# Kernel tuning notes

Hardware: AMD Instinct MI355X
Metric: run time of the kernel (lower is better)

The kernel has to match this reference:

```python
import jax, jax.numpy as jnp
import numpy as np

H = 2048          # hidden size
N_HEADS = 16
HEAD_DIM = H // N_HEADS   # 128
ATTN_SCALE = 8.0          # attention_scale > 1.0 -> custom max-subtract path
B, S = 2, 2048


def setup_inputs() -> dict:
    key = jax.random.key(0)
    k1, k2, k3, k4, k5 = jax.random.split(key, 5)
    hidden_states = jax.random.normal(k1, (B, S, H), dtype=jnp.float32)
    # causal left-to-right multiplicative mask, broadcast over batch and heads
    ltor_mask = jnp.tril(jnp.ones((S, S), dtype=jnp.float32))[None, None]
    std = 0.02
    W_qkv = jax.random.normal(k2, (H, 3 * H), dtype=jnp.float32) * std
    b_qkv = jnp.zeros((3 * H,), dtype=jnp.float32)
    W_out = jax.random.normal(k3, (H, H), dtype=jnp.float32) * std
    b_out = jnp.zeros((H,), dtype=jnp.float32)
    return {"hidden_states": hidden_states, "ltor_mask": ltor_mask,
            "W_qkv": W_qkv, "b_qkv": b_qkv, "W_out": W_out, "b_out": b_out}


def reference(hidden_states, ltor_mask, W_qkv, b_qkv, W_out, b_out):
    b, s, h = hidden_states.shape
    # fused QKV projection: [b, s, 3h]
    qkv = jnp.einsum('bsh,hk->bsk', hidden_states, W_qkv) + b_qkv
    q, k, v = jnp.split(qkv, 3, axis=-1)
    # [b, s, h] -> [b, n, s, hn]
    def to_heads(t):
        return t.reshape(b, s, N_HEADS, HEAD_DIM).transpose(0, 2, 1, 3)
    q, k, v = to_heads(q), to_heads(k), to_heads(v)
    # custom scale: q / sqrt(scale), k / sqrt(hn * scale)
    inv = 1.0 / (ATTN_SCALE * np.sqrt(np.float32(HEAD_DIM)))
    scores = jnp.einsum('bnqd,bnkd->bnqk', q, k) * jnp.float32(inv)
    # multiplicative mask BEFORE max-subtract (zeroes masked positions)
    scores = scores * ltor_mask
    # attention_scale > 1.0 path: subtract row max, re-multiply by scale
    scores = (scores - jnp.max(scores, axis=-1, keepdims=True)) * jnp.float32(ATTN_SCALE)
    # additive large-negative fill on masked entries
    scores = scores + jnp.float32(-65504.0) * (1.0 - ltor_mask)
    probs = jax.nn.softmax(scores, axis=-1)
    ctx = jnp.einsum('bnqk,bnkd->bnqd', probs, v)
    ctx = ctx.transpose(0, 2, 1, 3).reshape(b, s, h)
    out = jnp.einsum('bsh,hk->bsk', ctx, W_out) + b_out
    return out
```

## Files before the change

kernel.cpp:

```cpp
#include <hip/hip_runtime.h>

#define S_LEN 2048
#define HDIM  2048
#define NHEADS 16
#define DHEAD 128
#define BATCH 2
#define MROWS (BATCH * S_LEN)
#define QKVN  (3 * HDIM)

typedef _Float16 f16;
typedef _Float16 f16x8 __attribute__((ext_vector_type(8)));
typedef _Float16 f16x4 __attribute__((ext_vector_type(4)));
typedef float    f32x4 __attribute__((ext_vector_type(4)));
typedef float    f32x16 __attribute__((ext_vector_type(16)));

typedef const __attribute__((address_space(1))) void* gas_ptr;
typedef __attribute__((address_space(3))) void*       las_ptr;

#define MFMA16(a, b, c)  __builtin_amdgcn_mfma_f32_16x16x32_f16(a, b, c, 0, 0, 0)
#define MFMA32(a, b, c)  __builtin_amdgcn_mfma_f32_32x32x16_f16(a, b, c, 0, 0, 0)

__device__ __forceinline__ void gl_lds16(const f16* g, f16* lds_wave_base) {
#if defined(__has_builtin) && __has_builtin(__builtin_amdgcn_global_load_lds)
  __builtin_amdgcn_global_load_lds((gas_ptr)g, (las_ptr)lds_wave_base, 16, 0, 0);
#else
  int lane = threadIdx.x & 63;
  ((f16x8*)lds_wave_base)[lane] = *(const f16x8*)g;
#endif
}


__global__ __launch_bounds__(256) void cvt_blocked_kernel(const float* __restrict__ X,
                                                          f16* __restrict__ Xb) {
  int kt = blockIdx.x;
  int rt = blockIdx.y;
  int t = threadIdx.x;
  int m = t >> 1, half = t & 1;
  const float* src = X + (size_t)(rt * 128 + m) * HDIM + kt * 32 + half * 16;
  float4 v0 = ((const float4*)src)[0];
  float4 v1 = ((const float4*)src)[1];
  float4 v2 = ((const float4*)src)[2];
  float4 v3 = ((const float4*)src)[3];
  f16x8 a = {(f16)v0.x, (f16)v0.y, (f16)v0.z, (f16)v0.w,
             (f16)v1.x, (f16)v1.y, (f16)v1.z, (f16)v1.w};
  f16x8 b = {(f16)v2.x, (f16)v2.y, (f16)v2.z, (f16)v2.w,
             (f16)v3.x, (f16)v3.y, (f16)v3.z, (f16)v3.w};
  f16* dst = Xb + ((size_t)rt * 64 + kt) * 4096 + ((half * 2) * 128 + m) * 8;
  *(f16x8*)dst = a;
  *(f16x8*)(dst + 1024) = b;
}

__global__ __launch_bounds__(256) void transpose_cvt_blocked_kernel(
    const float* __restrict__ W, f16* __restrict__ Wb, int K, int N) {
  __shared__ float tile[64][65];
  int k0 = blockIdx.y * 64, n0 = blockIdx.x * 64;
  int tr = threadIdx.x >> 4;
  int tc = (threadIdx.x & 15) * 4;
  int KT = K >> 5;
#pragma unroll
  for (int rr = 0; rr < 4; ++rr) {
    int r = rr * 16 + tr;
    float4 v = *(const float4*)(W + (size_t)(k0 + r) * N + n0 + tc);
    tile[r][tc + 0] = v.x; tile[r][tc + 1] = v.y;
    tile[r][tc + 2] = v.z; tile[r][tc + 3] = v.w;
  }
  __syncthreads();
#pragma unroll
  for (int rr = 0; rr < 4; ++rr) {
    int r = rr * 16 + tr;
    int n = n0 + r;
    int kBase = k0 + tc;
    f16x4 o;
#pragma unroll
    for (int c = 0; c < 4; ++c) o[c] = (f16)tile[tc + c][r];
    int nt = n >> 7, nn = n & 127;
    int kt = kBase >> 5, kc = (kBase >> 3) & 3, j = kBase & 7;
    *(f16x4*)(Wb + ((size_t)nt * KT + kt) * 4096 + (kc * 128 + nn) * 8 + j) = o;
  }
}

template <int MODE>
__global__ __launch_bounds__(256) void gemm_kernel(const f16* __restrict__ Ablk,
                                                   const f16* __restrict__ Bblk,
                                                   const float* __restrict__ bias,
                                                   f16* __restrict__ Cpart,
                                                   f16* __restrict__ Qr,
                                                   f16* __restrict__ KB,
                                                   f16* __restrict__ VB,
                                                   int M, int N, int K) {
  __shared__ f16 As[4 * 128 * 8];
  __shared__ f16 Bs[4 * 128 * 8];
  int tid = threadIdx.x;
  int lane = tid & 63, w = tid >> 6;
  int lhi = lane >> 4, llo = lane & 15;
  int m0 = blockIdx.y * 128, n0 = blockIdx.x * 128;
  int wm = (w & 1) * 64, wn = (w >> 1) * 64;
  int KT = K >> 5;
  const f16* Ab = Ablk + (size_t)blockIdx.y * KT * 4096;
  const f16* Bb = Bblk + (size_t)blockIdx.x * KT * 4096;

  int ktBeg = 0, ktEnd = KT;
  if (MODE == 2) { int half = KT >> 1; ktBeg = blockIdx.z * half; ktEnd = ktBeg + half; }

  f32x4 acc[4][4];
#pragma unroll
  for (int i = 0; i < 4; ++i)
#pragma unroll
    for (int j = 0; j < 4; ++j) acc[i][j] = (f32x4){0.f, 0.f, 0.f, 0.f};

  for (int kt = ktBeg; kt < ktEnd; ++kt) {
    __syncthreads();
#pragma unroll
    for (int i2 = 0; i2 < 2; ++i2) {
      int Lw = i2 * 256 + w * 64;
      gl_lds16(Ab + (size_t)kt * 4096 + Lw * 8 + (lane * 8), As + Lw * 8);
      gl_lds16(Bb + (size_t)kt * 4096 + Lw * 8 + (lane * 8), Bs + Lw * 8);
    }
    __syncthreads();

    f16x8 af[4], bf[4];
#pragma unroll
    for (int i = 0; i < 4; ++i)
      af[i] = *(const f16x8*)(As + (lhi * 128 + wm + i * 16 + llo) * 8);
#pragma unroll
    for (int j = 0; j < 4; ++j)
      bf[j] = *(const f16x8*)(Bs + (lhi * 128 + wn + j * 16 + llo) * 8);
#pragma unroll
    for (int i = 0; i < 4; ++i)
#pragma unroll
      for (int j = 0; j < 4; ++j) acc[i][j] = MFMA16(af[i], bf[j], acc[i][j]);
  }

#pragma unroll
  for (int j = 0; j < 4; ++j) {
    int col = n0 + wn + j * 16 + llo;
    float bv = (MODE == 1) ? bias[col] : 0.f;
#pragma unroll
    for (int i = 0; i < 4; ++i) {
      int rowb = m0 + wm + i * 16 + lhi * 4;
      if (MODE == 2) {
        size_t zoff = (size_t)blockIdx.z * M * N;
#pragma unroll
        for (int r = 0; r < 4; ++r)
          Cpart[zoff + (size_t)(rowb + r) * N + col] = (f16)acc[i][j][r];
      } else {
        int region = n0 >> 11;
        if (region == 0) {
#pragma unroll
          for (int r = 0; r < 4; ++r)
            Qr[(size_t)(rowb + r) * HDIM + col] = (f16)(acc[i][j][r] + bv);
        } else if (region == 1) {
          int cK = col - HDIM;
          int hd = cK >> 7, d = cK & 127, g = d >> 3, dj = d & 7;
#pragma unroll
          for (int r = 0; r < 4; ++r) {
            int row = rowb + r;
            int b = row >> 11, s = row & 2047;
            int kt2 = s >> 6, key = s & 63;
            size_t addr = ((((size_t)(b * 16 + hd) * 32 + kt2) * 16 + g) * 64 + key) * 8 + dj;
            KB[addr] = (f16)(acc[i][j][r] + bv);
          }
        } else {
          int cV = col - 2 * HDIM;
          int hd = cV >> 7, d = cV & 127;
          int row = rowb;
          int b = row >> 11, s = row & 2047;
          int kt2 = s >> 6, key = s & 63;
          int kg = key >> 3, kj = key & 7;
          f16x4 pv = {(f16)(acc[i][j][0] + bv), (f16)(acc[i][j][1] + bv),
                      (f16)(acc[i][j][2] + bv), (f16)(acc[i][j][3] + bv)};
          size_t addr = ((((size_t)(b * 16 + hd) * 32 + kt2) * 8 + kg) * 128 + d) * 8 + kj;
          *(f16x4*)(VB + addr) = pv;
        }
      }
    }
  }
}

__global__ __launch_bounds__(256) void merge_out_kernel(const f16* __restrict__ Cpart,
                                                        const float* __restrict__ bias,
                                                        float* __restrict__ out) {
  int t = blockIdx.x * 256 + threadIdx.x;
  int col8 = (t & 255) * 8;
  int row = t >> 8;
  size_t base = (size_t)row * HDIM + col8;
  const size_t MN = (size_t)MROWS * HDIM;
  f16x8 a = *(const f16x8*)(Cpart + base);
  f16x8 b = *(const f16x8*)(Cpart + MN + base);
  float4 b0 = *(const float4*)(bias + col8);
  float4 b1 = *(const float4*)(bias + col8 + 4);
  float4 o0 = {(float)a[0] + (float)b[0] + b0.x, (float)a[1] + (float)b[1] + b0.y,
               (float)a[2] + (float)b[2] + b0.z, (float)a[3] + (float)b[3] + b0.w};
  float4 o1 = {(float)a[4] + (float)b[4] + b1.x, (float)a[5] + (float)b[5] + b1.y,
               (float)a[6] + (float)b[6] + b1.z, (float)a[7] + (float)b[7] + b1.w};
  *(float4*)(out + base) = o0;
  *(float4*)(out + base + 4) = o1;
}

__global__ __launch_bounds__(256, 2) void attn_kernel(const f16* __restrict__ Qr,
                                                      const f16* __restrict__ KB,
                                                      const f16* __restrict__ VB,
                                                      f16* __restrict__ Opart,
                                                      float* __restrict__ Lpart) {
  __shared__ f16 Ks[1024 * 8];
  __shared__ f16 Vs[1024 * 8];
  __shared__ f16 Ps[4][32 * 72];

  int tid = threadIdx.x, lane = tid & 63, w = tid >> 6;
  int l5 = lane & 31, hl = lane >> 5;
  int bh = blockIdx.y, b = bh >> 4, hd = bh & 15;
  int gx = blockIdx.x;

  int g, rem;
  if (gx < 4)       { g = 0; rem = gx; }
  else if (gx < 12) { g = 1; rem = gx - 4; }
  else if (gx < 24) { g = 2; rem = gx - 12; }
  else              { g = 3; rem = gx - 24; }
  int nseg = g + 1;
  int qt = g * 4 + rem / nseg;
  int seg = rem % nseg;
  int cnt = 2 * qt + 2;
  int kt0 = seg * cnt / nseg;
  int kt1 = (seg + 1) * cnt / nseg;

  int qbase = qt * 128 + w * 32;
  int qrow = qbase + l5;

  const f16* qp = Qr + (size_t)(b * S_LEN + qrow) * HDIM + hd * DHEAD + hl * 8;
  f16x8 qf[8];
#pragma unroll
  for (int s8 = 0; s8 < 8; ++s8) qf[s8] = *(const f16x8*)(qp + s8 * 16);

  f32x16 oac[4];
#pragma unroll
  for (int mt = 0; mt < 4; ++mt)
#pragma unroll
    for (int r = 0; r < 16; ++r) oac[mt][r] = 0.f;
  float rs = 0.f;

  const float C1 = 0.12752747419986393f;
  const float C2 = 11.541560327111708f;

  const f16* KBb = KB + (size_t)bh * 32 * 8192;
  const f16* VBb = VB + (size_t)bh * 32 * 8192;

  for (int kt = kt0; kt < kt1; ++kt) {
    __syncthreads();
    {
      const f16* Kt = KBb + (size_t)kt * 8192;
      const f16* Vt = VBb + (size_t)kt * 8192;
#pragma unroll
      for (int c = 0; c < 4; ++c) {
        int u0 = w * 256 + c * 64;
        gl_lds16(Kt + (size_t)(u0 + lane) * 8, Ks + u0 * 8);
        gl_lds16(Vt + (size_t)(u0 + lane) * 8, Vs + u0 * 8);
      }
    }
    __syncthreads();

    if (kt * 64 <= qbase + 31) {
      f32x16 sac[2];
#pragma unroll
      for (int mt = 0; mt < 2; ++mt)
#pragma unroll
        for (int r = 0; r < 16; ++r) sac[mt][r] = 0.f;
#pragma unroll
      for (int s8 = 0; s8 < 8; ++s8) {
#pragma unroll
        for (int mt = 0; mt < 2; ++mt) {
          f16x8 kf = *(const f16x8*)(Ks + ((s8 * 2 + hl) * 64 + mt * 32 + l5) * 8);
          sac[mt] = MFMA32(kf, qf[s8], sac[mt]);
        }
      }

      bool diag = (kt * 64 + 63 > qbase);
#pragma unroll
      for (int mt = 0; mt < 2; ++mt) {
#pragma unroll
        for (int g4 = 0; g4 < 4; ++g4) {
          f16x4 pk;
#pragma unroll
          for (int r = 0; r < 4; ++r) {
            int keyl = mt * 32 + g4 * 8 + hl * 4 + r;
            float p = __builtin_amdgcn_exp2f(fmaf(sac[mt][g4 * 4 + r], C1, -C2));
            if (diag && (kt * 64 + keyl > qrow)) p = 0.f;
            rs += p;
            pk[r] = (f16)p;
          }
          *(f16x4*)(&Ps[w][l5 * 72 + mt * 32 + g4 * 8 + hl * 4]) = pk;
        }
      }
      asm volatile("s_waitcnt lgkmcnt(0)" ::: "memory");

#pragma unroll
      for (int ks = 0; ks < 4; ++ks) {
        f16x8 pf = *(const f16x8*)(&Ps[w][l5 * 72 + ks * 16 + hl * 8]);
#pragma unroll
        for (int mt = 0; mt < 4; ++mt) {
          f16x8 vf = *(const f16x8*)(Vs + ((ks * 2 + hl) * 128 + mt * 32 + l5) * 8);
          oac[mt] = MFMA32(vf, pf, oac[mt]);
        }
      }
    }
  }

  float lsum = rs + __shfl_xor(rs, 32, 64);
  int lq = w * 32 + l5;
  size_t slot = (size_t)bh * 40 + gx;
  size_t ob = slot * (128 * DHEAD) + (size_t)lq * DHEAD;
#pragma unroll
  for (int mt = 0; mt < 4; ++mt) {
#pragma unroll
    for (int g4 = 0; g4 < 4; ++g4) {
      int d = mt * 32 + g4 * 8 + hl * 4;
      f16x4 ov = {(f16)oac[mt][g4 * 4 + 0], (f16)oac[mt][g4 * 4 + 1],
                  (f16)oac[mt][g4 * 4 + 2], (f16)oac[mt][g4 * 4 + 3]};
      *(f16x4*)(Opart + ob + d) = ov;
    }
  }
  if (hl == 0) Lpart[slot * 128 + lq] = lsum;
}

__global__ __launch_bounds__(256) void merge_kernel(const f16* __restrict__ Opart,
                                                    const float* __restrict__ Lpart,
                                                    f16* __restrict__ CTXb) {
  int t = blockIdx.x * 256 + threadIdx.x;
  int d8 = (t & 15) * 8;
  int q = (t >> 4) & 2047;
  int bh = t >> 15;
  int b = bh >> 4, hd = bh & 15;
  int qt = q >> 7, lq = q & 127;
  int g = qt >> 2;
  int nseg = g + 1;
  int gxbase = 2 * g * (g + 1) + (qt & 3) * nseg;
  size_t slot0 = (size_t)bh * 40 + gxbase;
  float acc[8];
#pragma unroll
  for (int j = 0; j < 8; ++j) acc[j] = 0.f;
  float l = 0.f;
  for (int s = 0; s < nseg; ++s) {
    l += Lpart[(slot0 + s) * 128 + lq];
    f16x8 a = *(const f16x8*)(Opart + (slot0 + s) * (128 * DHEAD) + (size_t)lq * DHEAD + d8);
#pragma unroll
    for (int j = 0; j < 8; ++j) acc[j] += (float)a[j];
  }
  float inv = 1.0f / l;
  f16x8 o;
#pragma unroll
  for (int j = 0; j < 8; ++j) o[j] = (f16)(acc[j] * inv);
  int row = b * S_LEN + q;
  int col = hd * DHEAD + d8;
  int rt = row >> 7, rr = row & 127;
  int kt = col >> 5, kc = (col >> 3) & 3;
  *(f16x8*)(CTXb + ((size_t)rt * 64 + kt) * 4096 + (kc * 128 + rr) * 8) = o;
}

extern "C" void kernel_launch(void* const* d_in, const int* in_sizes, int n_in,
                              void* d_out, int out_size, void* d_ws, size_t ws_size,
                              hipStream_t stream) {
  const float* X    = (const float*)d_in[0];
  const float* Wqkv = (const float*)d_in[2];
  const float* bqkv = (const float*)d_in[3];
  const float* Wout = (const float*)d_in[4];
  const float* bout = (const float*)d_in[5];
  float* out = (float*)d_out;

  char* ws = (char*)d_ws;
  f16* Xb    = (f16*)ws;  ws += (size_t)MROWS * HDIM * sizeof(f16);
  f16* Wqkvb = (f16*)ws;  ws += (size_t)QKVN * HDIM * sizeof(f16);
  f16* Woutb = (f16*)ws;  ws += (size_t)HDIM * HDIM * sizeof(f16);
  f16* Qr    = (f16*)ws;  ws += (size_t)MROWS * HDIM * sizeof(f16);
  f16* KB    = (f16*)ws;  ws += (size_t)32 * 32 * 8192 * sizeof(f16);
  f16* VB    = (f16*)ws;  ws += (size_t)32 * 32 * 8192 * sizeof(f16);
  f16* Opart = (f16*)ws;  ws += (size_t)32 * 40 * 128 * DHEAD * sizeof(f16);
  float* Lpart = (float*)ws;  ws += (size_t)32 * 40 * 128 * sizeof(float);
  f16* CTXb  = Xb;
  f16* Cpart = Opart;

  cvt_blocked_kernel<<<dim3(HDIM / 32, MROWS / 128), 256, 0, stream>>>(X, Xb);
  transpose_cvt_blocked_kernel<<<dim3(QKVN / 64, HDIM / 64), 256, 0, stream>>>(Wqkv, Wqkvb, HDIM, QKVN);
  transpose_cvt_blocked_kernel<<<dim3(HDIM / 64, HDIM / 64), 256, 0, stream>>>(Wout, Woutb, HDIM, HDIM);

  gemm_kernel<1><<<dim3(QKVN / 128, MROWS / 128), 256, 0, stream>>>(
      Xb, Wqkvb, bqkv, nullptr, Qr, KB, VB, MROWS, QKVN, HDIM);

  attn_kernel<<<dim3(40, 32), 256, 0, stream>>>(Qr, KB, VB, Opart, Lpart);

  merge_kernel<<<(32 * S_LEN * 16) / 256, 256, 0, stream>>>(Opart, Lpart, CTXb);

  gemm_kernel<2><<<dim3(HDIM / 128, MROWS / 128, 2), 256, 0, stream>>>(
      CTXb, Woutb, nullptr, Cpart, nullptr, nullptr, nullptr, MROWS, HDIM, HDIM);

  merge_out_kernel<<<(MROWS * HDIM / 8) / 256, 256, 0, stream>>>(Cpart, bout, out);
}
```

Baseline: 419.0 us.

## Double-buffer K/V tiles in attention and drop split-K in output projection

```diff
diff --git a/kernel.cpp b/kernel.cpp
--- a/kernel.cpp
+++ b/kernel.cpp
@@ -83,7 +83,7 @@
 __global__ __launch_bounds__(256) void gemm_kernel(const f16* __restrict__ Ablk,
                                                    const f16* __restrict__ Bblk,
                                                    const float* __restrict__ bias,
-                                                   f16* __restrict__ Cpart,
+                                                   float* __restrict__ Cout,
                                                    f16* __restrict__ Qr,
                                                    f16* __restrict__ KB,
                                                    f16* __restrict__ VB,
@@ -99,16 +99,13 @@
   const f16* Ab = Ablk + (size_t)blockIdx.y * KT * 4096;
   const f16* Bb = Bblk + (size_t)blockIdx.x * KT * 4096;
 
-  int ktBeg = 0, ktEnd = KT;
-  if (MODE == 2) { int half = KT >> 1; ktBeg = blockIdx.z * half; ktEnd = ktBeg + half; }
-
   f32x4 acc[4][4];
 #pragma unroll
   for (int i = 0; i < 4; ++i)
 #pragma unroll
     for (int j = 0; j < 4; ++j) acc[i][j] = (f32x4){0.f, 0.f, 0.f, 0.f};
 
-  for (int kt = ktBeg; kt < ktEnd; ++kt) {
+  for (int kt = 0; kt < KT; ++kt) {
     __syncthreads();
 #pragma unroll
     for (int i2 = 0; i2 < 2; ++i2) {
@@ -134,15 +131,14 @@
 #pragma unroll
   for (int j = 0; j < 4; ++j) {
     int col = n0 + wn + j * 16 + llo;
-    float bv = (MODE == 1) ? bias[col] : 0.f;
+    float bv = bias[col];
 #pragma unroll
     for (int i = 0; i < 4; ++i) {
       int rowb = m0 + wm + i * 16 + lhi * 4;
-      if (MODE == 2) {
-        size_t zoff = (size_t)blockIdx.z * M * N;
+      if (MODE == 0) {
 #pragma unroll
         for (int r = 0; r < 4; ++r)
-          Cpart[zoff + (size_t)(rowb + r) * N + col] = (f16)acc[i][j][r];
+          Cout[(size_t)(rowb + r) * N + col] = acc[i][j][r] + bv;
       } else {
         int region = n0 >> 11;
         if (region == 0) {
@@ -177,33 +173,13 @@
   }
 }
 
-__global__ __launch_bounds__(256) void merge_out_kernel(const f16* __restrict__ Cpart,
-                                                        const float* __restrict__ bias,
-                                                        float* __restrict__ out) {
-  int t = blockIdx.x * 256 + threadIdx.x;
-  int col8 = (t & 255) * 8;
-  int row = t >> 8;
-  size_t base = (size_t)row * HDIM + col8;
-  const size_t MN = (size_t)MROWS * HDIM;
-  f16x8 a = *(const f16x8*)(Cpart + base);
-  f16x8 b = *(const f16x8*)(Cpart + MN + base);
-  float4 b0 = *(const float4*)(bias + col8);
-  float4 b1 = *(const float4*)(bias + col8 + 4);
-  float4 o0 = {(float)a[0] + (float)b[0] + b0.x, (float)a[1] + (float)b[1] + b0.y,
-               (float)a[2] + (float)b[2] + b0.z, (float)a[3] + (float)b[3] + b0.w};
-  float4 o1 = {(float)a[4] + (float)b[4] + b1.x, (float)a[5] + (float)b[5] + b1.y,
-               (float)a[6] + (float)b[6] + b1.z, (float)a[7] + (float)b[7] + b1.w};
-  *(float4*)(out + base) = o0;
-  *(float4*)(out + base + 4) = o1;
-}
-
 __global__ __launch_bounds__(256, 2) void attn_kernel(const f16* __restrict__ Qr,
                                                       const f16* __restrict__ KB,
                                                       const f16* __restrict__ VB,
                                                       f16* __restrict__ Opart,
                                                       float* __restrict__ Lpart) {
-  __shared__ f16 Ks[1024 * 8];
-  __shared__ f16 Vs[1024 * 8];
+  __shared__ f16 Ks[2][1024 * 8];
+  __shared__ f16 Vs[2][1024 * 8];
   __shared__ f16 Ps[4][32 * 72];
 
   int tid = threadIdx.x, lane = tid & 63, w = tid >> 6;
@@ -244,19 +220,22 @@
   const f16* KBb = KB + (size_t)bh * 32 * 8192;
   const f16* VBb = VB + (size_t)bh * 32 * 8192;
 
+  auto stage = [&](int kt, int bi) {
+    const f16* Kt = KBb + (size_t)kt * 8192;
+    const f16* Vt = VBb + (size_t)kt * 8192;
+#pragma unroll
+    for (int c = 0; c < 4; ++c) {
+      int u0 = w * 256 + c * 64;
+      gl_lds16(Kt + (size_t)(u0 + lane) * 8, &Ks[bi][u0 * 8]);
+      gl_lds16(Vt + (size_t)(u0 + lane) * 8, &Vs[bi][u0 * 8]);
+    }
+  };
+
+  stage(kt0, 0);
   for (int kt = kt0; kt < kt1; ++kt) {
+    int cur = (kt - kt0) & 1;
     __syncthreads();
-    {
-      const f16* Kt = KBb + (size_t)kt * 8192;
-      const f16* Vt = VBb + (size_t)kt * 8192;
-#pragma unroll
-      for (int c = 0; c < 4; ++c) {
-        int u0 = w * 256 + c * 64;
-        gl_lds16(Kt + (size_t)(u0 + lane) * 8, Ks + u0 * 8);
-        gl_lds16(Vt + (size_t)(u0 + lane) * 8, Vs + u0 * 8);
-      }
-    }
-    __syncthreads();
+    if (kt + 1 < kt1) stage(kt + 1, cur ^ 1);
 
     if (kt * 64 <= qbase + 31) {
       f32x16 sac[2];
@@ -268,7 +247,7 @@
       for (int s8 = 0; s8 < 8; ++s8) {
 #pragma unroll
         for (int mt = 0; mt < 2; ++mt) {
-          f16x8 kf = *(const f16x8*)(Ks + ((s8 * 2 + hl) * 64 + mt * 32 + l5) * 8);
+          f16x8 kf = *(const f16x8*)(&Ks[cur][((s8 * 2 + hl) * 64 + mt * 32 + l5) * 8]);
           sac[mt] = MFMA32(kf, qf[s8], sac[mt]);
         }
       }
@@ -297,7 +276,7 @@
         f16x8 pf = *(const f16x8*)(&Ps[w][l5 * 72 + ks * 16 + hl * 8]);
 #pragma unroll
         for (int mt = 0; mt < 4; ++mt) {
-          f16x8 vf = *(const f16x8*)(Vs + ((ks * 2 + hl) * 128 + mt * 32 + l5) * 8);
+          f16x8 vf = *(const f16x8*)(&Vs[cur][((ks * 2 + hl) * 128 + mt * 32 + l5) * 8]);
           oac[mt] = MFMA32(vf, pf, oac[mt]);
         }
       }
@@ -375,7 +354,6 @@
   f16* Opart = (f16*)ws;  ws += (size_t)32 * 40 * 128 * DHEAD * sizeof(f16);
   float* Lpart = (float*)ws;  ws += (size_t)32 * 40 * 128 * sizeof(float);
   f16* CTXb  = Xb;
-  f16* Cpart = Opart;
 
   cvt_blocked_kernel<<<dim3(HDIM / 32, MROWS / 128), 256, 0, stream>>>(X, Xb);
   transpose_cvt_blocked_kernel<<<dim3(QKVN / 64, HDIM / 64), 256, 0, stream>>>(Wqkv, Wqkvb, HDIM, QKVN);
@@ -388,8 +366,6 @@
 
   merge_kernel<<<(32 * S_LEN * 16) / 256, 256, 0, stream>>>(Opart, Lpart, CTXb);
 
-  gemm_kernel<2><<<dim3(HDIM / 128, MROWS / 128, 2), 256, 0, stream>>>(
-      CTXb, Woutb, nullptr, Cpart, nullptr, nullptr, nullptr, MROWS, HDIM, HDIM);
-
-  merge_out_kernel<<<(MROWS * HDIM / 8) / 256, 256, 0, stream>>>(Cpart, bout, out);
-}
+  gemm_kernel<0><<<dim3(HDIM / 128, MROWS / 128), 256, 0, stream>>>(
+      CTXb, Woutb, bout, out, nullptr, nullptr, nullptr, MROWS, HDIM, HDIM);
+}
```

Result: slower. 452.6 us (+8.0%).
